# Optimization experiments

Hardware: AMD Instinct MI355X
Metric: run time of the kernel (lower is better)

## Reference

```python
import jax, jax.numpy as jnp
import numpy as np

ACTION_NS = [3, 3, 2, 4, 24]        # forward_back, left_right, jump, sneak_sprint, attack_...
RANGE_STARTS = [6, 8, 10, 11, 14]   # action_ranges starts (indices 0..5 are commit + camera ops)
N_ACTIONS = 37
LOGIT_DIM = 36
MIN_DELTA = 0.5 / 2**3
MAX_STEP = 20
MAX_CAMSTEP = 6
B, NUM_INPUT, HIDDEN = 32768, 1024, 2048
D_IN = NUM_INPUT + 4 + LOGIT_DIM


def setup_inputs():
    key = jax.random.key(0)
    ks = jax.random.split(key, 12)
    inp = {
        "fc_input": jax.random.normal(ks[0], (B, NUM_INPUT), jnp.float32),
        "camera": jax.random.normal(ks[1], (B, 2), jnp.float32),
        "rand_u": jax.random.uniform(ks[2], (B,), jnp.float32),
        "W1": (jax.random.normal(ks[3], (D_IN, HIDDEN), jnp.float32) / np.sqrt(D_IN)).astype(jnp.float32),
        "b1": jnp.zeros((HIDDEN,), jnp.float32),
        "W2": (jax.random.normal(ks[4], (HIDDEN, N_ACTIONS), jnp.float32) / np.sqrt(HIDDEN)).astype(jnp.float32),
        "b2": jnp.zeros((N_ACTIONS,), jnp.float32),
    }
    names = ["act_fb", "act_lr", "act_jp", "act_ss", "act_atk"]
    for i, (nm, n) in enumerate(zip(names, ACTION_NS)):
        inp[nm] = jax.random.randint(ks[5 + i], (B,), 0, n, jnp.int32)
    return inp


def _discretize_scan(camera, acts):
    # Faithful jax version of the 20-step no_grad target/input construction loop.
    nB = camera.shape[0]
    cam0, cam1 = camera[:, 0], camera[:, 1]

    def step(carry, _):
        ac, delta, rdac, dch, cam_steps, committed, norm = carry
        oh = [jax.nn.one_hot(r, n, dtype=jnp.float32) for r, n in zip(rdac, ACTION_NS)]
        inp_vec = jnp.concatenate([ac] + oh + [delta[:, None], dch.astype(jnp.float32)[:, None]], axis=1)  # [B,40]
        norm = norm + (~committed).astype(jnp.float32)
        commit = ((jnp.abs(cam0) < 1e-5) & (jnp.abs(cam1) < 1e-5)) | (cam_steps >= MAX_CAMSTEP)
        for r, a in zip(rdac, acts):
            commit = commit & (r == a)
        dac = jnp.zeros((nB,), jnp.int32)
        modified = commit
        new_rdac = []
        for r, a, rs in zip(rdac, acts, RANGE_STARTS):
            disc = (~modified) & (r != a)
            dac = jnp.where(disc & (a == 0), r - 1 + rs, jnp.where(disc, a - 1 + rs, dac))
            new_rdac.append(jnp.where(disc, a, r))
            modified = modified | disc
        d2 = delta * 2.0
        # NOTE: original torch code compares cam[:,1] against ac[:,0]; bug preserved.
        dmask = (~modified) & (~dch) & ((jnp.abs(cam0 - ac[:, 0]) > d2) | (jnp.abs(cam1 - ac[:, 0]) > d2))
        dac = jnp.where(dmask, 5, dac)
        delta = jnp.where(dmask, jnp.clip(d2, -0.5, 0.5), delta)
        modified = modified | dmask
        sx = jnp.where(cam0 < ac[:, 0], -1.0, 1.0)
        sy = jnp.where(cam1 < ac[:, 1], -1.0, 1.0)
        quad = jnp.where(sx < 0, jnp.where(sy < 0, 1, 3), jnp.where(sy < 0, 2, 4)).astype(jnp.int32)
        dac = jnp.where(~modified, quad, dac)
        move = jnp.stack([sx, sy], axis=1) * delta[:, None]
        ac = jnp.where((~modified)[:, None], ac + move, ac)
        delta = jnp.where(~modified, delta * 0.5, delta)
        dch = dch | (~modified)
        cam_steps = cam_steps + (~modified).astype(jnp.int32)
        committed = committed | commit
        return (ac, delta, tuple(new_rdac), dch, cam_steps, committed, norm), (inp_vec, dac)

    init = (jnp.zeros((nB, 2), jnp.float32),
            jnp.full((nB,), MIN_DELTA, jnp.float32),
            tuple(jnp.zeros((nB,), jnp.int32) for _ in ACTION_NS),
            jnp.zeros((nB,), bool),
            jnp.zeros((nB,), jnp.int32),
            jnp.zeros((nB,), bool),
            jnp.zeros((nB,), jnp.float32))
    carry, (all_inputs, all_dacs) = jax.lax.scan(step, init, None, length=MAX_STEP)
    return all_inputs, all_dacs, carry[-1]  # [T,B,40], [T,B], norm [B]


def reference(fc_input, camera, rand_u, W1, b1, W2, b2, act_fb, act_lr, act_jp, act_ss, act_atk):
    acts = (act_fb, act_lr, act_jp, act_ss, act_atk)
    all_inputs, all_dacs, norm = _discretize_scan(camera, acts)
    rand_sam = jnp.minimum((rand_u * norm).astype(jnp.int32), MAX_STEP - 1)  # sample an uncommitted step
    idx = jnp.arange(fc_input.shape[0])
    sel = jax.lax.stop_gradient(all_inputs[rand_sam, idx])  # [B,40]
    tgt = jax.lax.stop_gradient(all_dacs[rand_sam, idx])    # [B]
    x = jnp.concatenate([fc_input, sel], axis=1)
    h = x @ W1 + b1
    h = h * jax.nn.sigmoid(h)  # swish
    logits = h @ W2 + b2
    logp = jax.nn.log_softmax(logits, axis=-1)
    loss = -jnp.take_along_axis(logp, tgt[:, None], axis=1)[:, 0]  # per-sample CE (reduction='none')
    return loss
```

## Files before the change

### kernel.cpp

```cpp
#include <hip/hip_runtime.h>
#include <hip/hip_bf16.h>
#include <stdint.h>

#define B_ROWS 32768
#define NUM_IN 1024
#define D_PAD2 1088
#define HID    2048
#define NPAD   64

typedef __attribute__((ext_vector_type(8))) short bf16x8;
typedef __attribute__((ext_vector_type(4))) float f32x4;
typedef unsigned short ushort_t;

__device__ __forceinline__ unsigned short f2bf(float f){
  union { float f; uint32_t u; } x; x.f = f;
  uint32_t u = x.u;
  return (unsigned short)((u + 0x7FFFu + ((u >> 16) & 1u)) >> 16);
}

__device__ __forceinline__ void gload16(const void* g, void* l){
  __builtin_amdgcn_global_load_lds((const __attribute__((address_space(1))) void*)g,
                                   (__attribute__((address_space(3))) void*)l, 16, 0, 0);
}

__device__ __forceinline__ int disc_step(
    float cam0, float cam1, const int a[5],
    float& ac0, float& ac1, float& delta,
    int r[5], bool& dch, int& cam_steps, bool& committed, float& norm)
{
  const int RS[5] = {6, 8, 10, 11, 14};
  norm += committed ? 0.0f : 1.0f;
  bool commit = ((fabsf(cam0) < 1e-5f) && (fabsf(cam1) < 1e-5f)) || (cam_steps >= 6);
  #pragma unroll
  for (int i = 0; i < 5; ++i) commit = commit && (r[i] == a[i]);
  int dac = 0;
  bool modified = commit;
  #pragma unroll
  for (int i = 0; i < 5; ++i){
    bool disc = (!modified) && (r[i] != a[i]);
    if (disc){
      dac = (a[i] == 0) ? (r[i] - 1 + RS[i]) : (a[i] - 1 + RS[i]);
      r[i] = a[i];
      modified = true;
    }
  }
  float d2 = delta * 2.0f;
  bool dmask = (!modified) && (!dch) &&
               ((fabsf(cam0 - ac0) > d2) || (fabsf(cam1 - ac0) > d2));
  if (dmask){ dac = 5; delta = fminf(d2, 0.5f); modified = true; }
  if (!modified){
    float sx = (cam0 < ac0) ? -1.0f : 1.0f;
    float sy = (cam1 < ac1) ? -1.0f : 1.0f;
    dac = (sx < 0.0f) ? ((sy < 0.0f) ? 1 : 3) : ((sy < 0.0f) ? 2 : 4);
    ac0 += sx * delta; ac1 += sy * delta;
    delta *= 0.5f;
    dch = true;
    cam_steps += 1;
  }
  committed = committed || commit;
  return dac;
}

__global__ void k_prep(const float* __restrict__ fc, const float* __restrict__ W1,
                       const float* __restrict__ W2,
                       const float* __restrict__ camera, const float* __restrict__ rand_u,
                       const int* __restrict__ afb, const int* __restrict__ alr,
                       const int* __restrict__ ajp, const int* __restrict__ ass,
                       const int* __restrict__ aat,
                       unsigned short* __restrict__ xb, unsigned short* __restrict__ w1p,
                       unsigned short* __restrict__ w2t, int* __restrict__ tgt)
{
  __shared__ float lt[64][65];
  const int b = blockIdx.x;
  const int tid = threadIdx.x;
  if (b < 16384){
    int gid = b * 256 + tid;
    int row = gid >> 7;
    int c   = gid & 127;
    const float4* p = (const float4*)(fc + (size_t)row * NUM_IN + c * 8);
    float4 f0 = p[0], f1 = p[1];
    uint4 pk;
    pk.x = (uint32_t)f2bf(f0.x) | ((uint32_t)f2bf(f0.y) << 16);
    pk.y = (uint32_t)f2bf(f0.z) | ((uint32_t)f2bf(f0.w) << 16);
    pk.z = (uint32_t)f2bf(f1.x) | ((uint32_t)f2bf(f1.y) << 16);
    pk.w = (uint32_t)f2bf(f1.z) | ((uint32_t)f2bf(f1.w) << 16);
    *(uint4*)(xb + (size_t)row * D_PAD2 + c * 8) = pk;
    return;
  }
  if (b < 16928){
    const int bi = b - 16384;
    const int kt = bi % 17, nt = bi / 17;
    const int k0 = kt * 64, n0 = nt * 64;
    const int cgrp = nt >> 2, wn = nt & 3;
    const int c = tid & 63, rq = tid >> 6;
    #pragma unroll
    for (int rr = 0; rr < 16; ++rr){
      const int r = rr * 4 + rq;
      const int k = k0 + r;
      lt[r][c] = (k < 1064) ? W1[(size_t)k * HID + n0 + c] : 0.0f;
    }
    __syncthreads();
    #pragma unroll
    for (int s = 0; s < 2; ++s){
      const int idx = s * 256 + tid;
      const int ln = idx & 63, q = idx >> 6;
      const int lr2 = ln & 15, lg2 = ln >> 4;
      const int np = (q >> 2) * 32 + ((q >> 1) & 1) * 16 + lr2;
      const int kx = (q & 1) * 32 + lg2 * 8;
      uint4 pk;
      uint32_t w[4];
      #pragma unroll
      for (int e = 0; e < 4; ++e){
        unsigned short lo = f2bf(lt[kx + 2*e][np]);
        unsigned short hi = f2bf(lt[kx + 2*e + 1][np]);
        w[e] = (uint32_t)lo | ((uint32_t)hi << 16);
      }
      pk.x = w[0]; pk.y = w[1]; pk.z = w[2]; pk.w = w[3];
      *(uint4*)(w1p + (((size_t)cgrp*17 + kt) << 14) + (wn << 12) + q*512 + ln*8) = pk;
    }
    return;
  }
  if (b < 17440){
    int idx = (b - 16928) * 256 + tid;
    int n = idx >> 11;
    int k = idx & (HID - 1);
    float v = (n < 37) ? W2[(size_t)k * 37 + n] : 0.0f;
    w2t[idx] = f2bf(v);
    return;
  }
  int row = (b - 17440) * 256 + tid;
  float cam0 = camera[2*row], cam1 = camera[2*row + 1];
  int a[5] = { afb[row], alr[row], ajp[row], ass[row], aat[row] };

  float ac0 = 0.f, ac1 = 0.f, delta = 0.0625f, norm = 0.f;
  int r[5] = {0,0,0,0,0};
  bool dch = false, committed = false; int cam_steps = 0;
  for (int t = 0; t < 20; ++t)
    disc_step(cam0, cam1, a, ac0, ac1, delta, r, dch, cam_steps, committed, norm);

  int rs = (int)(rand_u[row] * norm);
  if (rs > 19) rs = 19;
  if (rs < 0) rs = 0;

  ac0 = 0.f; ac1 = 0.f; delta = 0.0625f; norm = 0.f;
  r[0]=r[1]=r[2]=r[3]=r[4]=0; dch = false; committed = false; cam_steps = 0;
  for (int t = 0; t < rs; ++t)
    disc_step(cam0, cam1, a, ac0, ac1, delta, r, dch, cam_steps, committed, norm);

  float vec[40];
  #pragma unroll
  for (int j = 0; j < 40; ++j) vec[j] = 0.0f;
  vec[0] = ac0; vec[1] = ac1;
  const int offs[5] = {2, 5, 8, 10, 14};
  #pragma unroll
  for (int i = 0; i < 5; ++i) vec[offs[i] + r[i]] = 1.0f;
  vec[38] = delta; vec[39] = dch ? 1.0f : 0.0f;

  int dac = disc_step(cam0, cam1, a, ac0, ac1, delta, r, dch, cam_steps, committed, norm);
  tgt[row] = dac;

  unsigned short* o = xb + (size_t)row * D_PAD2 + NUM_IN;
  #pragma unroll
  for (int j = 0; j < 40; ++j) o[j] = f2bf(vec[j]);
  #pragma unroll
  for (int j = 40; j < 64; ++j) o[j] = 0;
}


#define STAGE(REG, KT, HALF) do { \
    const ushort_t* s0_ = xb + (size_t)(brow + (HALF)*128 + srow) * D_PAD2 + ((KT) << 6) + scol; \
    gload16(s0_, lds + (REG) + (HALF)*8192 + t*8); \
    gload16(s0_ + (size_t)64 * D_PAD2, lds + (REG) + (HALF)*8192 + 4096 + t*8); \
  } while(0)

#define LDA_T(BO, MH) do { \
    _Pragma("unroll") for (int mi_ = 0; mi_ < 4; ++mi_) \
    _Pragma("unroll") for (int kk_ = 0; kk_ < 2; ++kk_) \
      aR[mi_][kk_] = *(const bf16x8*)(aBk[kk_] + (BO) + (((MH)*64 + mi_*16)*128)); \
  } while(0)

#define GLBH(BANK, KT, NH) do { \
    const ushort_t* bp_ = w1p + (((size_t)cgrp*17 + (KT)) << 14) + (wn << 12) + ((NH)*4)*512 + lane*8; \
    _Pragma("unroll") for (int ni_ = 0; ni_ < 2; ++ni_) \
    _Pragma("unroll") for (int kk_ = 0; kk_ < 2; ++kk_) \
      BANK[ni_][kk_] = *(const bf16x8*)(bp_ + (ni_*2 + kk_)*512); \
  } while(0)

#define MMA(MH, NH, BH) do { \
    __builtin_amdgcn_s_setprio(1); \
    _Pragma("unroll") for (int mi_ = 0; mi_ < 4; ++mi_) \
    _Pragma("unroll") for (int ni_ = 0; ni_ < 2; ++ni_) \
    _Pragma("unroll") for (int kk_ = 0; kk_ < 2; ++kk_) \
      acc[(MH)*4+mi_][(NH)*2+ni_] = __builtin_amdgcn_mfma_f32_16x16x32_bf16( \
          aR[mi_][kk_], BH[ni_][kk_], acc[(MH)*4+mi_][(NH)*2+ni_], 0, 0, 0); \
    __builtin_amdgcn_s_setprio(0); \
  } while(0)

#define BAR() __builtin_amdgcn_s_barrier()
#define WAIT_VM4() asm volatile("s_waitcnt vmcnt(4)" ::: "memory")
#define WAIT_VM0() asm volatile("s_waitcnt vmcnt(0)" ::: "memory")

__global__ __launch_bounds__(512, 2) void k_gemm1(const ushort_t* __restrict__ xb,
                                                  const ushort_t* __restrict__ w1p,
                                                  const ushort_t* __restrict__ w2t,
                                                  const float* __restrict__ b1,
                                                  float* __restrict__ pbuf)
{
  __shared__ ushort_t lds[65536];
  const int t = threadIdx.x;
  const int lane = t & 63;
  const int wid = t >> 6, wm = wid >> 2, wn = wid & 3;
  const int lr = lane & 15, lg = lane >> 4;

  const int bid = blockIdx.x;
  const int swz = (bid & 7) * 128 + (bid >> 3);
  const int brow = (swz >> 3) << 8;
  const int bcol = (swz & 7) << 8;
  const int cgrp = bcol >> 8;

  const int srow = t >> 3;
  const int scol = ((t & 7) ^ (srow & 7)) << 3;

  const int axor = lr & 7;
  const char* aBk[2];
  aBk[0] = (const char*)lds + (wm*128 + lr)*128 + (((0*4+lg)^axor) << 4);
  aBk[1] = (const char*)lds + (wm*128 + lr)*128 + (((1*4+lg)^axor) << 4);

  f32x4 acc[8][4] = {};
  bf16x8 aR[4][2];
  bf16x8 bH0[2][2], bH1[2][2];

  STAGE(0, 0, 0);  STAGE(0, 0, 1);
  GLBH(bH0, 0, 0); GLBH(bH1, 0, 1);
  STAGE(16384, 1, 0);  STAGE(16384, 1, 1);
  WAIT_VM4();
  BAR();

  #pragma unroll
  for (int tt = 0; tt < 17; ++tt){
    const int cbuf = (tt % 3) * 32768;
    const int sbo  = ((tt + 2) % 3) * 16384;
    const int st   = (tt + 2 <= 16) ? tt + 2 : 16;
    const int nk   = (tt + 1 <= 16) ? tt + 1 : 16;

    LDA_T(cbuf, 0);
    MMA(0, 0, bH0);
    MMA(0, 1, bH1);
    LDA_T(cbuf, 1);
    MMA(1, 0, bH0);
    GLBH(bH0, nk, 0);
    MMA(1, 1, bH1);
    GLBH(bH1, nk, 1);
    __builtin_amdgcn_sched_barrier(0);
    STAGE(sbo, st, 0);
    STAGE(sbo, st, 1);
    WAIT_VM4();
    BAR();
  }

  bf16x8 w2fA[4][4];
  #pragma unroll
  for (int ks = 0; ks < 4; ++ks)
    #pragma unroll
    for (int ni = 0; ni < 4; ++ni)
      w2fA[ks][ni] = *(const bf16x8*)(w2t + (size_t)(ni*16 + lr) * HID + bcol + ks*32 + lg*8);

  WAIT_VM0();
  BAR();

  float b1v[4];
  #pragma unroll
  for (int ni = 0; ni < 4; ++ni) b1v[ni] = b1[bcol + wn*64 + ni*16 + lr];

  #pragma unroll
  for (int mi = 0; mi < 8; ++mi){
    #pragma unroll
    for (int ni = 0; ni < 4; ++ni){
      const int col = wn*64 + ni*16 + lr;
      #pragma unroll
      for (int i2 = 0; i2 < 4; ++i2){
        const int row = wm*128 + mi*16 + lg*4 + i2;
        float v = acc[mi][ni][i2] + b1v[ni];
        float s = v / (1.0f + __expf(-v));
        const int chunk = (col >> 3) ^ (row & 7);
        lds[row*256 + chunk*8 + (col & 7)] = f2bf(s);
      }
    }
  }
  __syncthreads();

  bf16x8 w2fB[4][4];
  #pragma unroll
  for (int ks = 0; ks < 4; ++ks)
    #pragma unroll
    for (int ni = 0; ni < 4; ++ni)
      w2fB[ks][ni] = *(const bf16x8*)(w2t + (size_t)(ni*16 + lr) * HID + bcol + (ks+4)*32 + lg*8);

  const int rb = wid * 32;
  f32x4 acc2[2][4] = {};
  #pragma unroll
  for (int ks = 0; ks < 8; ++ks){
    bf16x8 a2[2];
    #pragma unroll
    for (int m = 0; m < 2; ++m){
      const int row = rb + m*16 + lr;
      a2[m] = *(const bf16x8*)(lds + row*256 + (((ks*4+lg) ^ (lr & 7)) << 3));
    }
    #pragma unroll
    for (int m = 0; m < 2; ++m)
      #pragma unroll
      for (int ni = 0; ni < 4; ++ni)
        acc2[m][ni] = __builtin_amdgcn_mfma_f32_16x16x32_bf16(
            a2[m], (ks < 4) ? w2fA[ks & 3][ni] : w2fB[ks & 3][ni], acc2[m][ni], 0, 0, 0);
  }

  const int cb = cgrp;
  #pragma unroll
  for (int m = 0; m < 2; ++m)
    #pragma unroll
    for (int ni = 0; ni < 4; ++ni)
      #pragma unroll
      for (int i2 = 0; i2 < 4; ++i2){
        const int r = brow + rb + m*16 + lg*4 + i2;
        pbuf[((size_t)cb << 21) + ((size_t)r << 6) + ni*16 + lr] = acc2[m][ni][i2];
      }
}

__global__ __launch_bounds__(256) void k_red(const float* __restrict__ pbuf,
                                             const float* __restrict__ b2,
                                             const int* __restrict__ tgt,
                                             float* __restrict__ loss)
{
  const int lane = threadIdx.x & 63, w = threadIdx.x >> 6;
  const int row0 = blockIdx.x * 128 + w * 32;
  const float bias = (lane < 37) ? b2[lane] : 0.0f;
  for (int i = 0; i < 32; ++i){
    const int r = row0 + i;
    float s = 0.0f;
    #pragma unroll
    for (int cb = 0; cb < 8; ++cb)
      s += pbuf[((size_t)cb << 21) + ((size_t)r << 6) + lane];
    float x = (lane < 37) ? (s + bias) : -1e30f;
    float m = x;
    #pragma unroll
    for (int off = 1; off < 64; off <<= 1) m = fmaxf(m, __shfl_xor(m, off, 64));
    float e = __expf(x - m);
    float se = e;
    #pragma unroll
    for (int off = 1; off < 64; off <<= 1) se += __shfl_xor(se, off, 64);
    const int tg = tgt[r];
    const float pick = __shfl(x, tg, 64);
    if (lane == 0) loss[r] = m + __logf(se) - pick;
  }
}

extern "C" void kernel_launch(void* const* d_in, const int* in_sizes, int n_in,
                              void* d_out, int out_size, void* d_ws, size_t ws_size,
                              hipStream_t stream)
{
  (void)in_sizes; (void)n_in; (void)out_size; (void)ws_size;
  const float* fc  = (const float*)d_in[0];
  const float* cam = (const float*)d_in[1];
  const float* ru  = (const float*)d_in[2];
  const float* W1  = (const float*)d_in[3];
  const float* b1  = (const float*)d_in[4];
  const float* W2  = (const float*)d_in[5];
  const float* b2  = (const float*)d_in[6];
  const int* afb = (const int*)d_in[7];
  const int* alr = (const int*)d_in[8];
  const int* ajp = (const int*)d_in[9];
  const int* ass = (const int*)d_in[10];
  const int* aat = (const int*)d_in[11];
  float* loss = (float*)d_out;

  char* ws = (char*)d_ws;
  unsigned short* xb  = (unsigned short*)(ws);
  unsigned short* w1p = (unsigned short*)(ws + 71303168);
  unsigned short* w2t = (unsigned short*)(ws + 75759616);
  int*            tgt = (int*)           (ws + 76021760);
  float*          pbuf= (float*)         (ws + 76152832);

  k_prep<<<17568, 256, 0, stream>>>(fc, W1, W2, cam, ru, afb, alr, ajp, ass, aat,
                                    xb, w1p, w2t, tgt);
  k_gemm1<<<(B_ROWS/256) * (HID/256), 512, 0, stream>>>(xb, w1p, w2t, b1, pbuf);
  k_red  <<<B_ROWS / 128, 256, 0, stream>>>(pbuf, b2, tgt, loss);
}
```

Measured before the change: 275.3 us.

## Replace pipelined 256x256 GEMM with simple 128x128 LDS-staged tiles and bf16 partials

The fused GEMM kernel drops its 256x256 tile with triple-buffered A staging and register-streamed prepacked W1. In its place is a 128x128 tile, 256-thread kernel that stages both A and a transposed W1 through LDS each k-step, with no overlap between loads and MFMA. W1 is now written transposed in row-major padded form, and the per-column-block logits partials are stored as bf16 across 16 blocks instead of fp32 across 8. The intent is likely higher occupancy and smaller partial traffic. The cost is the lost software pipelining, twice the memory reads of A/W per FLOP, and extra partial-sum precision loss.

```diff
diff --git a/kernel.cpp b/kernel.cpp
--- a/kernel.cpp
+++ b/kernel.cpp
@@ -16,6 +16,11 @@
   union { float f; uint32_t u; } x; x.f = f;
   uint32_t u = x.u;
   return (unsigned short)((u + 0x7FFFu + ((u >> 16) & 1u)) >> 16);
+}
+
+__device__ __forceinline__ float bf2f(unsigned short u){
+  union { uint32_t u; float f; } x; x.u = ((uint32_t)u) << 16;
+  return x.f;
 }
 
 __device__ __forceinline__ void gload16(const void* g, void* l){
@@ -67,7 +72,7 @@
                        const int* __restrict__ afb, const int* __restrict__ alr,
                        const int* __restrict__ ajp, const int* __restrict__ ass,
                        const int* __restrict__ aat,
-                       unsigned short* __restrict__ xb, unsigned short* __restrict__ w1p,
+                       unsigned short* __restrict__ xb, unsigned short* __restrict__ w1t,
                        unsigned short* __restrict__ w2t, int* __restrict__ tgt)
 {
   __shared__ float lt[64][65];
@@ -91,7 +96,6 @@
     const int bi = b - 16384;
     const int kt = bi % 17, nt = bi / 17;
     const int k0 = kt * 64, n0 = nt * 64;
-    const int cgrp = nt >> 2, wn = nt & 3;
     const int c = tid & 63, rq = tid >> 6;
     #pragma unroll
     for (int rr = 0; rr < 16; ++rr){
@@ -101,22 +105,9 @@
     }
     __syncthreads();
     #pragma unroll
-    for (int s = 0; s < 2; ++s){
-      const int idx = s * 256 + tid;
-      const int ln = idx & 63, q = idx >> 6;
-      const int lr2 = ln & 15, lg2 = ln >> 4;
-      const int np = (q >> 2) * 32 + ((q >> 1) & 1) * 16 + lr2;
-      const int kx = (q & 1) * 32 + lg2 * 8;
-      uint4 pk;
-      uint32_t w[4];
-      #pragma unroll
-      for (int e = 0; e < 4; ++e){
-        unsigned short lo = f2bf(lt[kx + 2*e][np]);
-        unsigned short hi = f2bf(lt[kx + 2*e + 1][np]);
-        w[e] = (uint32_t)lo | ((uint32_t)hi << 16);
-      }
-      pk.x = w[0]; pk.y = w[1]; pk.z = w[2]; pk.w = w[3];
-      *(uint4*)(w1p + (((size_t)cgrp*17 + kt) << 14) + (wn << 12) + q*512 + ln*8) = pk;
+    for (int rr = 0; rr < 16; ++rr){
+      const int r = rr * 4 + rq;
+      w1t[(size_t)(n0 + r) * D_PAD2 + k0 + c] = f2bf(lt[c][r]);
     }
     return;
   }
@@ -167,154 +158,119 @@
 }
 
 
-#define STAGE(REG, KT, HALF) do { \
-    const ushort_t* s0_ = xb + (size_t)(brow + (HALF)*128 + srow) * D_PAD2 + ((KT) << 6) + scol; \
-    gload16(s0_, lds + (REG) + (HALF)*8192 + t*8); \
-    gload16(s0_ + (size_t)64 * D_PAD2, lds + (REG) + (HALF)*8192 + 4096 + t*8); \
-  } while(0)
-
-#define LDA_T(BO, MH) do { \
-    _Pragma("unroll") for (int mi_ = 0; mi_ < 4; ++mi_) \
-    _Pragma("unroll") for (int kk_ = 0; kk_ < 2; ++kk_) \
-      aR[mi_][kk_] = *(const bf16x8*)(aBk[kk_] + (BO) + (((MH)*64 + mi_*16)*128)); \
-  } while(0)
-
-#define GLBH(BANK, KT, NH) do { \
-    const ushort_t* bp_ = w1p + (((size_t)cgrp*17 + (KT)) << 14) + (wn << 12) + ((NH)*4)*512 + lane*8; \
-    _Pragma("unroll") for (int ni_ = 0; ni_ < 2; ++ni_) \
-    _Pragma("unroll") for (int kk_ = 0; kk_ < 2; ++kk_) \
-      BANK[ni_][kk_] = *(const bf16x8*)(bp_ + (ni_*2 + kk_)*512); \
-  } while(0)
-
-#define MMA(MH, NH, BH) do { \
-    __builtin_amdgcn_s_setprio(1); \
-    _Pragma("unroll") for (int mi_ = 0; mi_ < 4; ++mi_) \
-    _Pragma("unroll") for (int ni_ = 0; ni_ < 2; ++ni_) \
-    _Pragma("unroll") for (int kk_ = 0; kk_ < 2; ++kk_) \
-      acc[(MH)*4+mi_][(NH)*2+ni_] = __builtin_amdgcn_mfma_f32_16x16x32_bf16( \
-          aR[mi_][kk_], BH[ni_][kk_], acc[(MH)*4+mi_][(NH)*2+ni_], 0, 0, 0); \
-    __builtin_amdgcn_s_setprio(0); \
-  } while(0)
-
-#define BAR() __builtin_amdgcn_s_barrier()
-#define WAIT_VM4() asm volatile("s_waitcnt vmcnt(4)" ::: "memory")
-#define WAIT_VM0() asm volatile("s_waitcnt vmcnt(0)" ::: "memory")
-
-__global__ __launch_bounds__(512, 2) void k_gemm1(const ushort_t* __restrict__ xb,
-                                                  const ushort_t* __restrict__ w1p,
+#define BAR() __syncthreads()
+
+__global__ __launch_bounds__(256, 3) void k_gemm1(const ushort_t* __restrict__ xb,
+                                                  const ushort_t* __restrict__ w1t,
                                                   const ushort_t* __restrict__ w2t,
                                                   const float* __restrict__ b1,
-                                                  float* __restrict__ pbuf)
-{
-  __shared__ ushort_t lds[65536];
+                                                  ushort_t* __restrict__ pbuf)
+{
+  __shared__ ushort_t lds[16384];
   const int t = threadIdx.x;
   const int lane = t & 63;
-  const int wid = t >> 6, wm = wid >> 2, wn = wid & 3;
+  const int wid = t >> 6;
+  const int wm = wid >> 1, wn = wid & 1;
   const int lr = lane & 15, lg = lane >> 4;
 
   const int bid = blockIdx.x;
-  const int swz = (bid & 7) * 128 + (bid >> 3);
-  const int brow = (swz >> 3) << 8;
-  const int bcol = (swz & 7) << 8;
-  const int cgrp = bcol >> 8;
-
-  const int srow = t >> 3;
-  const int scol = ((t & 7) ^ (srow & 7)) << 3;
+  const int swz = (bid & 7) * 512 + (bid >> 3);
+  const int brow = (swz >> 4) << 7;
+  const int bcol = (swz & 15) << 7;
+  const int cb   = swz & 15;
 
   const int axor = lr & 7;
   const char* aBk[2];
-  aBk[0] = (const char*)lds + (wm*128 + lr)*128 + (((0*4+lg)^axor) << 4);
-  aBk[1] = (const char*)lds + (wm*128 + lr)*128 + (((1*4+lg)^axor) << 4);
-
-  f32x4 acc[8][4] = {};
-  bf16x8 aR[4][2];
-  bf16x8 bH0[2][2], bH1[2][2];
-
-  STAGE(0, 0, 0);  STAGE(0, 0, 1);
-  GLBH(bH0, 0, 0); GLBH(bH1, 0, 1);
-  STAGE(16384, 1, 0);  STAGE(16384, 1, 1);
-  WAIT_VM4();
-  BAR();
-
-  #pragma unroll
-  for (int tt = 0; tt < 17; ++tt){
-    const int cbuf = (tt % 3) * 32768;
-    const int sbo  = ((tt + 2) % 3) * 16384;
-    const int st   = (tt + 2 <= 16) ? tt + 2 : 16;
-    const int nk   = (tt + 1 <= 16) ? tt + 1 : 16;
-
-    LDA_T(cbuf, 0);
-    MMA(0, 0, bH0);
-    MMA(0, 1, bH1);
-    LDA_T(cbuf, 1);
-    MMA(1, 0, bH0);
-    GLBH(bH0, nk, 0);
-    MMA(1, 1, bH1);
-    GLBH(bH1, nk, 1);
-    __builtin_amdgcn_sched_barrier(0);
-    STAGE(sbo, st, 0);
-    STAGE(sbo, st, 1);
-    WAIT_VM4();
+  const char* bBk[2];
+  aBk[0] = (const char*)lds + (wm*64 + lr)*128 + (((0 + lg) ^ axor) << 4);
+  aBk[1] = (const char*)lds + (wm*64 + lr)*128 + (((4 + lg) ^ axor) << 4);
+  bBk[0] = (const char*)lds + 16384 + (wn*64 + lr)*128 + (((0 + lg) ^ axor) << 4);
+  bBk[1] = (const char*)lds + 16384 + (wn*64 + lr)*128 + (((4 + lg) ^ axor) << 4);
+
+  f32x4 acc[4][4] = {};
+  bf16x8 aR[4][2], bR[4][2];
+
+  for (int kt = 0; kt < 17; ++kt){
+    #pragma unroll
+    for (int s = 0; s < 4; ++s){
+      const int sr = s*32 + (t >> 3);
+      const int sc = ((t & 7) ^ (sr & 7)) << 3;
+      gload16(xb  + (size_t)(brow + sr) * D_PAD2 + (kt << 6) + sc, lds + s*2048 + t*8);
+      gload16(w1t + (size_t)(bcol + sr) * D_PAD2 + (kt << 6) + sc, lds + 8192 + s*2048 + t*8);
+    }
     BAR();
-  }
-
-  bf16x8 w2fA[4][4];
-  #pragma unroll
-  for (int ks = 0; ks < 4; ++ks)
+
+    #pragma unroll
+    for (int mi = 0; mi < 4; ++mi)
+      #pragma unroll
+      for (int kk = 0; kk < 2; ++kk)
+        aR[mi][kk] = *(const bf16x8*)(aBk[kk] + mi*16*128);
     #pragma unroll
     for (int ni = 0; ni < 4; ++ni)
-      w2fA[ks][ni] = *(const bf16x8*)(w2t + (size_t)(ni*16 + lr) * HID + bcol + ks*32 + lg*8);
-
-  WAIT_VM0();
-  BAR();
+      #pragma unroll
+      for (int kk = 0; kk < 2; ++kk)
+        bR[ni][kk] = *(const bf16x8*)(bBk[kk] + ni*16*128);
+
+    __builtin_amdgcn_s_setprio(1);
+    #pragma unroll
+    for (int mi = 0; mi < 4; ++mi)
+      #pragma unroll
+      for (int ni = 0; ni < 4; ++ni)
+        #pragma unroll
+        for (int kk = 0; kk < 2; ++kk)
+          acc[mi][ni] = __builtin_amdgcn_mfma_f32_16x16x32_bf16(
+              aR[mi][kk], bR[ni][kk], acc[mi][ni], 0, 0, 0);
+    __builtin_amdgcn_s_setprio(0);
+    BAR();
+  }
 
   float b1v[4];
   #pragma unroll
   for (int ni = 0; ni < 4; ++ni) b1v[ni] = b1[bcol + wn*64 + ni*16 + lr];
 
   #pragma unroll
-  for (int mi = 0; mi < 8; ++mi){
+  for (int mi = 0; mi < 4; ++mi){
     #pragma unroll
     for (int ni = 0; ni < 4; ++ni){
       const int col = wn*64 + ni*16 + lr;
       #pragma unroll
       for (int i2 = 0; i2 < 4; ++i2){
-        const int row = wm*128 + mi*16 + lg*4 + i2;
+        const int row = wm*64 + mi*16 + lg*4 + i2;
         float v = acc[mi][ni][i2] + b1v[ni];
         float s = v / (1.0f + __expf(-v));
-        const int chunk = (col >> 3) ^ (row & 7);
-        lds[row*256 + chunk*8 + (col & 7)] = f2bf(s);
+        const int c = col >> 3;
+        lds[row*128 + ((c ^ (row & 7)) << 3) + (col & 7)] = f2bf(s);
       }
     }
   }
-  __syncthreads();
-
-  bf16x8 w2fB[4][4];
+  BAR();
+
+  bf16x8 w2f[4][4];
   #pragma unroll
   for (int ks = 0; ks < 4; ++ks)
     #pragma unroll
     for (int ni = 0; ni < 4; ++ni)
-      w2fB[ks][ni] = *(const bf16x8*)(w2t + (size_t)(ni*16 + lr) * HID + bcol + (ks+4)*32 + lg*8);
+      w2f[ks][ni] = *(const bf16x8*)(w2t + (size_t)(ni*16 + lr) * HID + bcol + ks*32 + lg*8);
 
   const int rb = wid * 32;
   f32x4 acc2[2][4] = {};
   #pragma unroll
-  for (int ks = 0; ks < 8; ++ks){
+  for (int ks = 0; ks < 4; ++ks){
     bf16x8 a2[2];
     #pragma unroll
     for (int m = 0; m < 2; ++m){
       const int row = rb + m*16 + lr;
-      a2[m] = *(const bf16x8*)(lds + row*256 + (((ks*4+lg) ^ (lr & 7)) << 3));
+      const int c = ks*4 + lg;
+      a2[m] = *(const bf16x8*)(lds + row*128 + ((c ^ (row & 7)) << 3));
     }
     #pragma unroll
     for (int m = 0; m < 2; ++m)
       #pragma unroll
       for (int ni = 0; ni < 4; ++ni)
         acc2[m][ni] = __builtin_amdgcn_mfma_f32_16x16x32_bf16(
-            a2[m], (ks < 4) ? w2fA[ks & 3][ni] : w2fB[ks & 3][ni], acc2[m][ni], 0, 0, 0);
-  }
-
-  const int cb = cgrp;
+            a2[m], w2f[ks][ni], acc2[m][ni], 0, 0, 0);
+  }
+
   #pragma unroll
   for (int m = 0; m < 2; ++m)
     #pragma unroll
@@ -322,11 +278,11 @@
       #pragma unroll
       for (int i2 = 0; i2 < 4; ++i2){
         const int r = brow + rb + m*16 + lg*4 + i2;
-        pbuf[((size_t)cb << 21) + ((size_t)r << 6) + ni*16 + lr] = acc2[m][ni][i2];
+        pbuf[((size_t)cb << 21) + ((size_t)r << 6) + ni*16 + lr] = f2bf(acc2[m][ni][i2]);
       }
 }
 
-__global__ __launch_bounds__(256) void k_red(const float* __restrict__ pbuf,
+__global__ __launch_bounds__(256) void k_red(const ushort_t* __restrict__ pbuf,
                                              const float* __restrict__ b2,
                                              const int* __restrict__ tgt,
                                              float* __restrict__ loss)
@@ -338,8 +294,8 @@
     const int r = row0 + i;
     float s = 0.0f;
     #pragma unroll
-    for (int cb = 0; cb < 8; ++cb)
-      s += pbuf[((size_t)cb << 21) + ((size_t)r << 6) + lane];
+    for (int cbk = 0; cbk < 16; ++cbk)
+      s += bf2f(pbuf[((size_t)cbk << 21) + ((size_t)r << 6) + lane]);
     float x = (lane < 37) ? (s + bias) : -1e30f;
     float m = x;
     #pragma unroll
@@ -375,13 +331,13 @@
 
   char* ws = (char*)d_ws;
   unsigned short* xb  = (unsigned short*)(ws);
-  unsigned short* w1p = (unsigned short*)(ws + 71303168);
+  unsigned short* w1t = (unsigned short*)(ws + 71303168);
   unsigned short* w2t = (unsigned short*)(ws + 75759616);
   int*            tgt = (int*)           (ws + 76021760);
-  float*          pbuf= (float*)         (ws + 76152832);
+  unsigned short* pbuf= (unsigned short*)(ws + 76152832);
 
   k_prep<<<17568, 256, 0, stream>>>(fc, W1, W2, cam, ru, afb, alr, ajp, ass, aat,
-                                    xb, w1p, w2t, tgt);
-  k_gemm1<<<(B_ROWS/256) * (HID/256), 512, 0, stream>>>(xb, w1p, w2t, b1, pbuf);
+                                    xb, w1t, w2t, tgt);
+  k_gemm1<<<(B_ROWS/128) * (HID/128), 256, 0, stream>>>(xb, w1t, w2t, b1, pbuf);
   k_red  <<<B_ROWS / 128, 256, 0, stream>>>(pbuf, b2, tgt, loss);
 }
```

Measured after the change: 267.4 us. -2.9%, faster.
